# Kernel tuning notes

Hardware: AMD Instinct MI355X
Metric: run time of the kernel (lower is better)

The kernel has to match this reference:

```python
import jax, jax.numpy as jnp
import numpy as np

TIME_WINDOW = 80
TC_IN = 17.452274
TD = 0.0
TC1 = TC2 = TC3 = 20.0
V_INIT = 1.0
NOT_FIRED = 9999.0


def setup_inputs() -> dict:
    key = jax.random.key(0)
    k0, k1, k2, k3, k4, k5, k6 = jax.random.split(key, 7)
    B = 4096
    return {
        "input_image": jax.random.uniform(k0, (B, 1, 28, 28), dtype=jnp.float32),
        "conv1_w": jax.random.normal(k1, (12, 1, 5, 5), dtype=jnp.float32) * 0.3,
        "conv1_b": jax.random.normal(k2, (12,), dtype=jnp.float32) * 0.1,
        "conv2_w": jax.random.normal(k3, (64, 12, 5, 5), dtype=jnp.float32) * 0.1,
        "conv2_b": jax.random.normal(k4, (64,), dtype=jnp.float32) * 0.1,
        "fc1_w": jax.random.normal(k5, (1024, 10), dtype=jnp.float32) * 0.1,
        "fc1_b": jax.random.normal(k6, (10,), dtype=jnp.float32) * 0.1,
    }


def _conv(x, w, b):
    y = jax.lax.conv_general_dilated(x, w, (1, 1), "VALID",
                                     dimension_numbers=("NCHW", "OIHW", "NCHW"))
    return y + b[None, :, None, None]


def _max_pool2x2(x):
    return jax.lax.reduce_window(x, -jnp.inf, jax.lax.max,
                                 (1, 1, 2, 2), (1, 1, 2, 2), "VALID")


def _neuron(v_mem, has_fired, curr, t, tc):
    # TemporalNeuron: integrate, dynamic threshold v_init*exp(-(t-td)/tc), fire once.
    v_mem = v_mem + curr
    v_th = V_INIT * jnp.exp(-(t - TD) / tc)
    fire = (v_mem >= v_th) & (~has_fired) & (v_th > 1e-5)
    return v_mem, has_fired | fire, fire.astype(v_mem.dtype)


def _ttfs_pool(x, fired_mask):
    # Min-time pooling: only the earliest spike in each 2x2 window passes.
    p = _max_pool2x2(x)
    valid = (p > 0.5) & (~fired_mask)
    return valid.astype(x.dtype), fired_mask | valid


def reference(input_image, conv1_w, conv1_b, conv2_w, conv2_b, fc1_w, fc1_b):
    B = input_image.shape[0]
    # Inputs are in [0,1) so no /255 branch (pixel.max() <= 1.05 in original).
    pixel = jnp.clip(input_image, 1e-5, None)
    spike_times_in = jnp.ceil(jnp.clip(-TC_IN * jnp.log(pixel), 0.0, None))

    init = (
        jnp.zeros((B, 12, 24, 24), jnp.float32), jnp.zeros((B, 12, 24, 24), bool),
        jnp.zeros((B, 12, 12, 12), bool),
        jnp.zeros((B, 64, 8, 8), jnp.float32), jnp.zeros((B, 64, 8, 8), bool),
        jnp.zeros((B, 64, 4, 4), bool),
        jnp.zeros((B, 10), jnp.float32), jnp.zeros((B, 10), bool),
        jnp.full((B, 10), NOT_FIRED, jnp.float32),
    )

    def step(carry, t):
        v1, f1, pm1, v2, f2, pm2, v3, f3, out_times = carry
        mask_in = (jnp.abs(t - spike_times_in) < 0.5).astype(jnp.float32)
        v1, f1, spk1 = _neuron(v1, f1, _conv(mask_in, conv1_w, conv1_b), t, TC1)
        spk1_p, pm1 = _ttfs_pool(spk1, pm1)
        v2, f2, spk2 = _neuron(v2, f2, _conv(spk1_p, conv2_w, conv2_b), t, TC2)
        spk2_p, pm2 = _ttfs_pool(spk2, pm2)
        flat = spk2_p.transpose(0, 2, 3, 1).reshape(B, -1)  # NHWC flatten, matches torch permute
        v3, f3, spk3 = _neuron(v3, f3, flat @ fc1_w + fc1_b, t, TC3)
        out_times = jnp.where((spk3 > 0.5) & (out_times == NOT_FIRED), t, out_times)
        return (v1, f1, pm1, v2, f2, pm2, v3, f3, out_times), None

    ts = jnp.arange(TIME_WINDOW, dtype=jnp.float32)
    carry, _ = jax.lax.scan(step, init, ts)
    return carry[-1]
```

## Files before the change

kernel.cpp:

```cpp
#include <hip/hip_runtime.h>
#include <math.h>

#define NOT_FIREDf 9999.0f
typedef float f32x2 __attribute__((ext_vector_type(2)));

#define PKADD(ACC, W) asm("v_pk_add_f32 %0, %0, %1" : "+v"(ACC) : "v"(W))

__global__ void w2_pad_kernel(const float* __restrict__ w2, float* __restrict__ w2p) {
    int idx = blockIdx.x * 256 + threadIdx.x;
    if (idx >= 74176) return;
    if (idx >= 72960) { w2p[idx] = 0.0f; return; }
    int co = idx & 63;
    int r = idx >> 6;
    int rx = r % 19;
    int q = r / 19;
    int dy = q % 5;
    int ci = q / 5;
    int dx = rx - 7;
    w2p[idx] = ((unsigned)dx < 5u) ? w2[(co * 12 + ci) * 25 + dy * 5 + dx] : 0.0f;
}

#define GATHER_V1(S, Y, X) do {                                              \
    const int dy_ = py - (Y), dx_ = px - (X);                                \
    if (((unsigned)dy_ < 5u) & ((unsigned)dx_ < 5u)) {                       \
        const f32x2* wp_ = (const f32x2*)&w1s[(dy_ * 5 + dx_) * 12];         \
        PKADD(v1r[S][0], wp_[0]); PKADD(v1r[S][1], wp_[1]);                  \
        PKADD(v1r[S][2], wp_[2]); PKADD(v1r[S][3], wp_[3]);                  \
        PKADD(v1r[S][4], wp_[4]); PKADD(v1r[S][5], wp_[5]);                  \
    } } while (0)

#define P1EVENT(PK) do {                                                     \
    const int py = (int)((PK) >> 8);                                         \
    const int px = (int)((PK) & 255u);                                       \
    GATHER_V1(0, y0, x0);                                                    \
    GATHER_V1(1, y1, x1);                                                    \
    if (has2) GATHER_V1(2, y2, x2);                                          \
  } while (0)

#define CHECK_V1F(S, Y, X) do {                                              \
    const f32x2* bp_ = (const f32x2*)b1s;                                    \
    PKADD(v1r[S][0], bp_[0]); PKADD(v1r[S][1], bp_[1]);                      \
    PKADD(v1r[S][2], bp_[2]); PKADD(v1r[S][3], bp_[3]);                      \
    PKADD(v1r[S][4], bp_[4]); PKADD(v1r[S][5], bp_[5]);                      \
    float m_ = fmaxf(fmaxf(fmaxf(v1r[S][0].x, v1r[S][0].y),                  \
                           fmaxf(v1r[S][1].x, v1r[S][1].y)),                 \
                     fmaxf(fmaxf(v1r[S][2].x, v1r[S][2].y),                  \
                           fmaxf(v1r[S][3].x, v1r[S][3].y)));                \
    m_ = fmaxf(m_, fmaxf(fmaxf(v1r[S][4].x, v1r[S][4].y),                    \
                         fmaxf(v1r[S][5].x, v1r[S][5].y)));                  \
    if (m_ >= th) {                                                          \
        _Pragma("unroll")                                                    \
        for (int jj = 0; jj < 6; ++jj) {                                     \
            _Pragma("unroll")                                                \
            for (int el = 0; el < 2; ++el) {                                 \
                const float v_ = el ? v1r[S][jj].y : v1r[S][jj].x;           \
                if (v_ >= th) {                                              \
                    if (el) v1r[S][jj].y = -__builtin_inff();                \
                    else    v1r[S][jj].x = -__builtin_inff();                \
                    const int c_ = jj * 2 + el;                              \
                    const int pyp_ = (Y) >> 1, pxp_ = (X) >> 1;              \
                    const int bidx_ = ((c_ * 144 + pyp_ * 12 + pxp_) << 2)   \
                                    | (((Y) & 1) << 1) | ((X) & 1);          \
                    f1b[bidx_] = (unsigned char)t;                           \
                }                                                            \
            }                                                                \
        }                                                                    \
    } } while (0)

#define P2_ONE(PA) do {                                                      \
    const int dA_ = (((PA) >> 4) & 15) - oyb_s;                              \
    if ((unsigned)dA_ < 6u) {                                                \
        const int ci_ = (PA) >> 8;                                           \
        const int px_ = (PA) & 15;                                           \
        const float* r0_ = (dA_ <= 4) ? (w2p + (ci_ * 5 + dA_) * 1216) : zrow; \
        const float* r1_ = (dA_ >= 1) ? (w2p + (ci_ * 5 + dA_ - 1) * 1216) : zrow; \
        const float* q0_ = r0_ + (px_ + 7) * 64 + lane;                      \
        const float* q1_ = r1_ + (px_ + 7) * 64 + lane;                      \
        f32x2 la_[4];                                                        \
        _Pragma("unroll")                                                    \
        for (int j = 0; j < 4; ++j) { la_[j].x = q0_[-(j * 64)]; la_[j].y = q1_[-(j * 64)]; } \
        _Pragma("unroll")                                                    \
        for (int j = 0; j < 4; ++j) PKADD(v2r2[j], la_[j]);                  \
        _Pragma("unroll")                                                    \
        for (int j = 0; j < 4; ++j) { la_[j].x = q0_[-((4 + j) * 64)]; la_[j].y = q1_[-((4 + j) * 64)]; } \
        _Pragma("unroll")                                                    \
        for (int j = 0; j < 4; ++j) PKADD(v2r2[4 + j], la_[j]);              \
    } } while (0)

__device__ __forceinline__ unsigned min4b(unsigned w) {
    unsigned a = w & 255u, b = (w >> 8) & 255u, c = (w >> 16) & 255u, d = w >> 24;
    unsigned m0 = a < b ? a : b;
    unsigned m1 = c < d ? c : d;
    return m0 < m1 ? m0 : m1;
}

template <int USE_T>
__global__ void __launch_bounds__(256, 4)
snn_sim_kernel(const float* __restrict__ img,
               const float* __restrict__ w1g,
               const float* __restrict__ b1g,
               const float* __restrict__ b2g,
               const float* __restrict__ w2raw,
               const float* __restrict__ w2p,
               const float* __restrict__ fcw,
               const float* __restrict__ b3g,
               float* __restrict__ out) {
    const int bimg = blockIdx.x;
    const int tid  = threadIdx.x;
    const int lane = tid & 63;
    const int wv   = tid >> 6;
    const int oyb_s = __builtin_amdgcn_readfirstlane(wv) * 2;
    const int wv_s  = oyb_s >> 1;

    __shared__ __align__(16) float w1s[300];
    __shared__ __align__(8)  float b1s[12];
    __shared__ float th_lds[80];
    __shared__ unsigned char  stin[784];
    __shared__ unsigned short evlist[784];
    __shared__ unsigned short off[81];
    __shared__ unsigned short o1[81];
    __shared__ unsigned int   hist[80];
    __shared__ unsigned int   f1w[1728];
    __shared__ __align__(8) unsigned short ev1s[1728];
    __shared__ unsigned char  e2t[1024];

    unsigned char* f1b = (unsigned char*)f1w;

    for (int i = tid; i < 300; i += 256) {
        int k = i / 12, c = i - k * 12;
        w1s[i] = w1g[c * 25 + k];
    }
    if (tid < 12) b1s[tid] = b1g[tid];
    if (tid < 80) {
        float xa = (0.0f - (float)tid) / 20.0f;
        th_lds[tid] = (float)exp((double)xa);
        hist[tid] = 0u;
    }
    for (int i = tid; i < 1728; i += 256) f1w[i] = 0xFFFFFFFFu;
    for (int i = tid; i < 1024; i += 256) e2t[i] = 0xFF;
    for (int i = tid; i < 784; i += 256) {
        float p = img[bimg * 784 + i];
        p = fmaxf(p, 1e-5f);
        float lg = (float)log((double)p);
        float s = ceilf(fmaxf(-17.452274f * lg, 0.0f));
        stin[i] = (unsigned char)(int)fminf(s, 255.0f);
    }
    __syncthreads();
    for (int i = tid; i < 784; i += 256) {
        int t = stin[i];
        if (t < 80) atomicAdd(&hist[t], 1u);
    }
    __syncthreads();
    if (tid == 0) {
        unsigned int acc = 0;
        for (int t = 0; t < 80; ++t) { off[t] = (unsigned short)acc; acc += hist[t]; }
        off[80] = (unsigned short)acc;
    }
    __syncthreads();
    if (tid < 80) {
        int k = off[tid];
        for (int i = 0; i < 784; ++i)
            if ((int)stin[i] == tid) {
                int py = i / 28;
                evlist[k++] = (unsigned short)((py << 8) | (i - py * 28));
            }
    }
    if (tid >= 80 && tid < 160) hist[tid - 80] = 0u;
    __syncthreads();

    {
        f32x2 v1r[3][6];
#pragma unroll
        for (int s = 0; s < 3; ++s)
#pragma unroll
            for (int j = 0; j < 6; ++j) v1r[s][j] = (f32x2){0.0f, 0.0f};

        const int y0 = tid / 24,  x0 = tid - y0 * 24;
        const int p1i = tid + 256;
        const int y1 = p1i / 24,  x1 = p1i - y1 * 24;
        const int has2 = (tid < 64);
        const int p2i = tid + 512;
        const int y2 = p2i / 24,  x2 = p2i - y2 * 24;

        for (int t = 0; t < 80; ++t) {
            const float th = th_lds[t];
            const int e0 = off[t], e1t = off[t + 1];
            int e = e0;
            for (; e + 4 <= e1t; e += 4) {
                const unsigned a0 = evlist[e];
                const unsigned a1 = evlist[e + 1];
                const unsigned a2 = evlist[e + 2];
                const unsigned a3 = evlist[e + 3];
                P1EVENT(a0); P1EVENT(a1); P1EVENT(a2); P1EVENT(a3);
            }
            for (; e < e1t; ++e) { const unsigned a = evlist[e]; P1EVENT(a); }
            CHECK_V1F(0, y0, x0);
            CHECK_V1F(1, y1, x1);
            if (has2) CHECK_V1F(2, y2, x2);
        }
    }
    __syncthreads();

    for (int p = tid; p < 1728; p += 256) {
        unsigned tm = min4b(f1w[p]);
        if (tm < 80u) atomicAdd(&hist[tm], 1u);
    }
    __syncthreads();
    if (tid == 0) {
        unsigned acc = 0;
        for (int t = 0; t < 80; ++t) { o1[t] = (unsigned short)acc; acc += hist[t]; }
        o1[80] = (unsigned short)acc;
    }
    __syncthreads();
    if (tid < 80) {
        int k = o1[tid];
        for (int p = 0; p < 1728; ++p) {
            if (min4b(f1w[p]) == (unsigned)tid) {
                int c = p / 144;
                int rem = p - c * 144;
                int py = rem / 12;
                int px = rem - py * 12;
                ev1s[k++] = (unsigned short)((c << 8) | (py << 4) | px);
            }
        }
    }
    if (tid >= 80 && tid < 160) hist[tid - 80] = 0u;
    __syncthreads();

    {
        f32x2 v2r2[8];
#pragma unroll
        for (int j = 0; j < 8; ++j) v2r2[j] = (f32x2){0.0f, 0.0f};
        const float b2v = b2g[lane];
        const f32x2 b2p = (f32x2){b2v, b2v};
        const float* zrow = w2p + 72960;
        unsigned fired2 = 0u;

        for (int t = 0; t < 80; ++t) {
            const float th = th_lds[t];
            const int e0 = o1[t], e1t = o1[t + 1];
            if (USE_T) {
                int e = e0;
                for (; e + 4 <= e1t; e += 4) {
                    const int p0 = __builtin_amdgcn_readfirstlane((int)ev1s[e]);
                    const int p1 = __builtin_amdgcn_readfirstlane((int)ev1s[e + 1]);
                    const int p2 = __builtin_amdgcn_readfirstlane((int)ev1s[e + 2]);
                    const int p3 = __builtin_amdgcn_readfirstlane((int)ev1s[e + 3]);
                    P2_ONE(p0); P2_ONE(p1); P2_ONE(p2); P2_ONE(p3);
                }
                for (; e < e1t; ++e) {
                    const int p0 = __builtin_amdgcn_readfirstlane((int)ev1s[e]);
                    P2_ONE(p0);
                }
            } else {
                for (int e = e0; e < e1t; ++e) {
                    const int pk = __builtin_amdgcn_readfirstlane((int)ev1s[e]);
                    const int dy0 = ((pk >> 4) & 15) - oyb_s;
                    if ((unsigned)dy0 >= 6u) continue;
                    const int ci = pk >> 8;
                    const int px = pk & 15;
                    const int dy1 = dy0 - 1;
                    const unsigned colm = ((0x1Fu << px) >> 4) & 0xFFu;
                    const unsigned m0 = ((unsigned)dy0 < 5u) ? colm : 0u;
                    const unsigned m1 = ((unsigned)dy1 < 5u) ? colm : 0u;
                    const int dy0c = dy0 < 0 ? 0 : (dy0 > 4 ? 4 : dy0);
                    const int dy1c = dy1 < 0 ? 0 : (dy1 > 4 ? 4 : dy1);
                    const float* cb = w2raw + lane * 300 + ci * 25;
                    const float* r0 = cb + dy0c * 5;
                    const float* r1 = cb + dy1c * 5;
#pragma unroll
                    for (int j = 0; j < 8; ++j) {
                        const int dx = px - j;
                        const int dxc = dx < 0 ? 0 : (dx > 4 ? 4 : dx);
                        v2r2[j].x = fmaf(r0[dxc], ((m0 >> j) & 1u) ? 1.0f : 0.0f, v2r2[j].x);
                        v2r2[j].y = fmaf(r1[dxc], ((m1 >> j) & 1u) ? 1.0f : 0.0f, v2r2[j].y);
                    }
                }
            }
            PKADD(v2r2[0], b2p); PKADD(v2r2[1], b2p);
            PKADD(v2r2[2], b2p); PKADD(v2r2[3], b2p);
            PKADD(v2r2[4], b2p); PKADD(v2r2[5], b2p);
            PKADD(v2r2[6], b2p); PKADD(v2r2[7], b2p);
            float m2 = fmaxf(fmaxf(fmaxf(v2r2[0].x, v2r2[0].y), fmaxf(v2r2[1].x, v2r2[1].y)),
                             fmaxf(fmaxf(v2r2[2].x, v2r2[2].y), fmaxf(v2r2[3].x, v2r2[3].y)));
            m2 = fmaxf(m2, fmaxf(fmaxf(fmaxf(v2r2[4].x, v2r2[4].y), fmaxf(v2r2[5].x, v2r2[5].y)),
                                 fmaxf(fmaxf(v2r2[6].x, v2r2[6].y), fmaxf(v2r2[7].x, v2r2[7].y))));
            if (m2 >= th) {
#pragma unroll
                for (int j = 0; j < 8; ++j) {
#pragma unroll
                    for (int el = 0; el < 2; ++el) {
                        const float v = el ? v2r2[j].y : v2r2[j].x;
                        if (v >= th) {
                            if (el) v2r2[j].y = -__builtin_inff();
                            else    v2r2[j].x = -__builtin_inff();
                            const unsigned bit = 1u << (j >> 1);
                            if (!(fired2 & bit)) {
                                fired2 |= bit;
                                const int p2 = (wv_s * 4 + (j >> 1)) * 64 + lane;
                                e2t[p2] = (unsigned char)t;
                            }
                        }
                    }
                }
            }
        }
    }
    __syncthreads();

    for (int p = tid; p < 1024; p += 256) {
        unsigned t = e2t[p];
        if (t < 80u) atomicAdd(&hist[t], 1u);
    }
    __syncthreads();
    if (tid == 0) {
        unsigned acc = 0;
        for (int t = 0; t < 80; ++t) { off[t] = (unsigned short)acc; acc += hist[t]; }
        off[80] = (unsigned short)acc;
    }
    __syncthreads();
    if (tid < 80) {
        int k = off[tid];
        for (int p = 0; p < 1024; ++p)
            if ((int)e2t[p] == tid) ev1s[k++] = (unsigned short)p;
    }
    __syncthreads();

    if (tid < 10) {
        const float b3v = b3g[tid];
        float v = 0.0f;
        float ot = NOT_FIREDf;
        for (int t = 0; t < 80; ++t) {
            float acc = 0.0f;
            for (int e = off[t]; e < off[t + 1]; ++e)
                acc += fcw[(int)ev1s[e] * 10 + tid];
            v += acc + b3v;
            if (ot == NOT_FIREDf && v >= th_lds[t]) ot = (float)t;
        }
        out[bimg * 10 + tid] = ot;
    }
}

extern "C" void kernel_launch(void* const* d_in, const int* in_sizes, int n_in,
                              void* d_out, int out_size, void* d_ws, size_t ws_size,
                              hipStream_t stream) {
    const float* img = (const float*)d_in[0];
    const float* w1  = (const float*)d_in[1];
    const float* b1  = (const float*)d_in[2];
    const float* w2  = (const float*)d_in[3];
    const float* b2  = (const float*)d_in[4];
    const float* fcw = (const float*)d_in[5];
    const float* b3  = (const float*)d_in[6];
    float* out = (float*)d_out;

    const int B = in_sizes[0] / (28 * 28);

    float* w2p = (float*)d_ws;
    const int use_t = (ws_size >= 74176u * sizeof(float)) ? 1 : 0;
    if (use_t) {
        hipLaunchKernelGGL(w2_pad_kernel, dim3(290), dim3(256), 0, stream, w2, w2p);
        hipLaunchKernelGGL(snn_sim_kernel<1>, dim3(B), dim3(256), 0, stream,
                           img, w1, b1, b2, w2, w2p, fcw, b3, out);
    } else {
        hipLaunchKernelGGL(snn_sim_kernel<0>, dim3(B), dim3(256), 0, stream,
                           img, w1, b1, b2, w2, w2p, fcw, b3, out);
    }
}
```

Before: 2.873 ms.

## Skip zero-row loads in conv2 events, vectorize event reads, cache pooled spike times

```diff
diff --git a/kernel.cpp b/kernel.cpp
--- a/kernel.cpp
+++ b/kernel.cpp
@@ -8,8 +8,7 @@
 
 __global__ void w2_pad_kernel(const float* __restrict__ w2, float* __restrict__ w2p) {
     int idx = blockIdx.x * 256 + threadIdx.x;
-    if (idx >= 74176) return;
-    if (idx >= 72960) { w2p[idx] = 0.0f; return; }
+    if (idx >= 72960) return;
     int co = idx & 63;
     int r = idx >> 6;
     int rx = r % 19;
@@ -72,19 +71,34 @@
     if ((unsigned)dA_ < 6u) {                                                \
         const int ci_ = (PA) >> 8;                                           \
         const int px_ = (PA) & 15;                                           \
-        const float* r0_ = (dA_ <= 4) ? (w2p + (ci_ * 5 + dA_) * 1216) : zrow; \
-        const float* r1_ = (dA_ >= 1) ? (w2p + (ci_ * 5 + dA_ - 1) * 1216) : zrow; \
-        const float* q0_ = r0_ + (px_ + 7) * 64 + lane;                      \
-        const float* q1_ = r1_ + (px_ + 7) * 64 + lane;                      \
-        f32x2 la_[4];                                                        \
-        _Pragma("unroll")                                                    \
-        for (int j = 0; j < 4; ++j) { la_[j].x = q0_[-(j * 64)]; la_[j].y = q1_[-(j * 64)]; } \
-        _Pragma("unroll")                                                    \
-        for (int j = 0; j < 4; ++j) PKADD(v2r2[j], la_[j]);                  \
-        _Pragma("unroll")                                                    \
-        for (int j = 0; j < 4; ++j) { la_[j].x = q0_[-((4 + j) * 64)]; la_[j].y = q1_[-((4 + j) * 64)]; } \
-        _Pragma("unroll")                                                    \
-        for (int j = 0; j < 4; ++j) PKADD(v2r2[4 + j], la_[j]);              \
+        const float* base_ = w2p + (px_ + 7) * 64 + lane;                    \
+        if (dA_ == 0) {                                                      \
+            const float* q0_ = base_ + (ci_ * 5) * 1216;                     \
+            float lx_[8];                                                    \
+            _Pragma("unroll")                                                \
+            for (int j = 0; j < 8; ++j) lx_[j] = q0_[-(j * 64)];             \
+            _Pragma("unroll")                                                \
+            for (int j = 0; j < 8; ++j) v2r2[j].x += lx_[j];                 \
+        } else if (dA_ == 5) {                                               \
+            const float* q1_ = base_ + (ci_ * 5 + 4) * 1216;                 \
+            float ly_[8];                                                    \
+            _Pragma("unroll")                                                \
+            for (int j = 0; j < 8; ++j) ly_[j] = q1_[-(j * 64)];             \
+            _Pragma("unroll")                                                \
+            for (int j = 0; j < 8; ++j) v2r2[j].y += ly_[j];                 \
+        } else {                                                             \
+            const float* q0_ = base_ + (ci_ * 5 + dA_) * 1216;               \
+            const float* q1_ = q0_ - 1216;                                   \
+            f32x2 la_[4];                                                    \
+            _Pragma("unroll")                                                \
+            for (int j = 0; j < 4; ++j) { la_[j].x = q0_[-(j * 64)]; la_[j].y = q1_[-(j * 64)]; } \
+            _Pragma("unroll")                                                \
+            for (int j = 0; j < 4; ++j) PKADD(v2r2[j], la_[j]);              \
+            _Pragma("unroll")                                                \
+            for (int j = 0; j < 4; ++j) { la_[j].x = q0_[-((4 + j) * 64)]; la_[j].y = q1_[-((4 + j) * 64)]; } \
+            _Pragma("unroll")                                                \
+            for (int j = 0; j < 4; ++j) PKADD(v2r2[4 + j], la_[j]);          \
+        }                                                                    \
     } } while (0)
 
 __device__ __forceinline__ unsigned min4b(unsigned w) {
@@ -116,11 +130,12 @@
     __shared__ __align__(8)  float b1s[12];
     __shared__ float th_lds[80];
     __shared__ unsigned char  stin[784];
-    __shared__ unsigned short evlist[784];
+    __shared__ __align__(8) unsigned short evlist[784];
     __shared__ unsigned short off[81];
     __shared__ unsigned short o1[81];
     __shared__ unsigned int   hist[80];
     __shared__ unsigned int   f1w[1728];
+    __shared__ unsigned char  tmb1[1728];
     __shared__ __align__(8) unsigned short ev1s[1728];
     __shared__ unsigned char  e2t[1024];
 
@@ -178,19 +193,21 @@
         const int y0 = tid / 24,  x0 = tid - y0 * 24;
         const int p1i = tid + 256;
         const int y1 = p1i / 24,  x1 = p1i - y1 * 24;
-        const int has2 = (tid < 64);
-        const int p2i = tid + 512;
+        const int has2 = (tid >= 192);
+        const int p2i = tid + 320;
         const int y2 = p2i / 24,  x2 = p2i - y2 * 24;
 
         for (int t = 0; t < 80; ++t) {
             const float th = th_lds[t];
             const int e0 = off[t], e1t = off[t + 1];
             int e = e0;
+            for (; e < e1t && (e & 3); ++e) { const unsigned a = evlist[e]; P1EVENT(a); }
             for (; e + 4 <= e1t; e += 4) {
-                const unsigned a0 = evlist[e];
-                const unsigned a1 = evlist[e + 1];
-                const unsigned a2 = evlist[e + 2];
-                const unsigned a3 = evlist[e + 3];
+                const unsigned long long q = *(const unsigned long long*)&evlist[e];
+                const unsigned a0 = (unsigned)(q & 0xFFFFu);
+                const unsigned a1 = (unsigned)((q >> 16) & 0xFFFFu);
+                const unsigned a2 = (unsigned)((q >> 32) & 0xFFFFu);
+                const unsigned a3 = (unsigned)(q >> 48);
                 P1EVENT(a0); P1EVENT(a1); P1EVENT(a2); P1EVENT(a3);
             }
             for (; e < e1t; ++e) { const unsigned a = evlist[e]; P1EVENT(a); }
@@ -203,6 +220,7 @@
 
     for (int p = tid; p < 1728; p += 256) {
         unsigned tm = min4b(f1w[p]);
+        tmb1[p] = (unsigned char)tm;
         if (tm < 80u) atomicAdd(&hist[tm], 1u);
     }
     __syncthreads();
@@ -215,7 +233,7 @@
     if (tid < 80) {
         int k = o1[tid];
         for (int p = 0; p < 1728; ++p) {
-            if (min4b(f1w[p]) == (unsigned)tid) {
+            if ((int)tmb1[p] == tid) {
                 int c = p / 144;
                 int rem = p - c * 144;
                 int py = rem / 12;
@@ -233,7 +251,6 @@
         for (int j = 0; j < 8; ++j) v2r2[j] = (f32x2){0.0f, 0.0f};
         const float b2v = b2g[lane];
         const f32x2 b2p = (f32x2){b2v, b2v};
-        const float* zrow = w2p + 72960;
         unsigned fired2 = 0u;
 
         for (int t = 0; t < 80; ++t) {
@@ -356,9 +373,9 @@
     const int B = in_sizes[0] / (28 * 28);
 
     float* w2p = (float*)d_ws;
-    const int use_t = (ws_size >= 74176u * sizeof(float)) ? 1 : 0;
+    const int use_t = (ws_size >= 72960u * sizeof(float)) ? 1 : 0;
     if (use_t) {
-        hipLaunchKernelGGL(w2_pad_kernel, dim3(290), dim3(256), 0, stream, w2, w2p);
+        hipLaunchKernelGGL(w2_pad_kernel, dim3(285), dim3(256), 0, stream, w2, w2p);
         hipLaunchKernelGGL(snn_sim_kernel<1>, dim3(B), dim3(256), 0, stream,
                            img, w1, b1, b2, w2, w2p, fcw, b3, out);
     } else {
```

Measured after the change: 2.787 ms (median of 2 runs). 1.03x faster.
